# Kernel optimization log

Measured on AMD Instinct MI355X. Metric: run time of the kernel, lower is better.

## Reference

```python
import jax, jax.numpy as jnp
import numpy as np

RES = 300
NC = 48
N_PTS = 1_000_000


def _bilinear2d(params, gx, gy):
    """params: (C,R,R); gx,gy: (N,) in [-1,1]. grid_sample align_corners=True,
    gx indexes width (last axis), gy indexes height."""
    C, R, _ = params.shape
    px = (gx + 1.0) * 0.5 * (R - 1)
    py = (gy + 1.0) * 0.5 * (R - 1)
    x0f = jnp.floor(px)
    y0f = jnp.floor(py)
    wx = px - x0f
    wy = py - y0f
    x0 = jnp.clip(x0f.astype(jnp.int32), 0, R - 1)
    x1 = jnp.clip(x0 + 1, 0, R - 1)
    y0 = jnp.clip(y0f.astype(jnp.int32), 0, R - 1)
    y1 = jnp.clip(y0 + 1, 0, R - 1)
    f00 = params[:, y0, x0]  # (C,N)
    f01 = params[:, y0, x1]
    f10 = params[:, y1, x0]
    f11 = params[:, y1, x1]
    return (f00 * (1 - wx) * (1 - wy) + f01 * wx * (1 - wy)
            + f10 * (1 - wx) * wy + f11 * wx * wy)


def _linear1d(params, gy):
    """params: (C,R) (line grid with width 1, x-coord fixed at 0); gy: (N,)."""
    C, R = params.shape
    py = (gy + 1.0) * 0.5 * (R - 1)
    y0f = jnp.floor(py)
    wy = py - y0f
    y0 = jnp.clip(y0f.astype(jnp.int32), 0, R - 1)
    y1 = jnp.clip(y0 + 1, 0, R - 1)
    return params[:, y0] * (1 - wy) + params[:, y1] * wy  # (C,N)


def setup_inputs() -> dict:
    key = jax.random.key(0)
    k1, k2, k3 = jax.random.split(key, 3)
    x = jax.random.uniform(k1, (N_PTS, 3), dtype=jnp.float32)
    plane_params = 0.1 * jax.random.normal(k2, (3, NC, RES, RES), dtype=jnp.float32)
    line_params = 0.1 * jax.random.normal(k3, (3, NC, RES, 1), dtype=jnp.float32)
    return {"x": x, "plane_params": plane_params, "line_params": line_params}


def reference(x, plane_params, line_params):
    N = x.shape[0]
    xs = 2.0 * x - 1.0  # (N,3)
    # grid_sample grid is (x_coord, y_coord): plane pairs [0,1],[0,2],[1,2]
    gx = jnp.stack([xs[:, 0], xs[:, 0], xs[:, 1]])  # (3,N) width coord
    gy = jnp.stack([xs[:, 1], xs[:, 2], xs[:, 2]])  # (3,N) height coord
    gl = jnp.stack([xs[:, 2], xs[:, 1], xs[:, 0]])  # (3,N) line coord
    plane_f = jax.vmap(_bilinear2d)(plane_params, gx, gy)      # (3,C,N)
    line_f = jax.vmap(_linear1d)(line_params[..., 0], gl)      # (3,C,N)
    feats = (plane_f * line_f).reshape(3 * NC, N).T            # (N, 3C)
    return feats
```

## Files before the change

kernel.cpp:

```cpp
#include <hip/hip_runtime.h>
#include <hip/hip_fp16.h>

#define RES 300
#define NC 48
#define RES2 (RES * RES)
#define NBINS 32768
#define TPP 12

typedef float f32x4 __attribute__((ext_vector_type(4)));
typedef unsigned int u32x4 __attribute__((ext_vector_type(4)));

struct alignas(8) h4 { __half2 h[2]; };

__device__ __forceinline__ int clampi(int v, int lo, int hi) {
    return v < lo ? lo : (v > hi ? hi : v);
}

__device__ __forceinline__ unsigned spread5(unsigned v) {
    v &= 31u;
    v = (v | (v << 8)) & 0x100Fu;
    v = (v | (v << 4)) & 0x10C3u;
    v = (v | (v << 2)) & 0x1249u;
    return v;
}

__device__ __forceinline__ unsigned morton_key(float a, float b, float c) {
    int ca = clampi((int)(a * 32.0f), 0, 31);
    int cb = clampi((int)(b * 32.0f), 0, 31);
    int cc = clampi((int)(c * 32.0f), 0, 31);
    return spread5((unsigned)ca) | (spread5((unsigned)cb) << 1) | (spread5((unsigned)cc) << 2);
}


__global__ __launch_bounds__(256) void tp_planes_kernel(const float* __restrict__ in,
                                                        __half* __restrict__ out) {
    unsigned idx = blockIdx.x * 256u + threadIdx.x;
    if (idx >= 3u * RES2) return;
    unsigned p  = idx / RES2;
    unsigned yx = idx - p * RES2;
    const float* src = in + (size_t)p * NC * RES2 + yx;
    unsigned short v[NC];
#pragma unroll
    for (int c = 0; c < NC; ++c) {
        __half h = __float2half(src[(size_t)c * RES2]);
        v[c] = *reinterpret_cast<unsigned short*>(&h);
    }
    u32x4* dst = reinterpret_cast<u32x4*>(out + (size_t)idx * NC);
#pragma unroll
    for (int i = 0; i < 6; ++i) {
        u32x4 w;
        w.x = (unsigned)v[8 * i + 0] | ((unsigned)v[8 * i + 1] << 16);
        w.y = (unsigned)v[8 * i + 2] | ((unsigned)v[8 * i + 3] << 16);
        w.z = (unsigned)v[8 * i + 4] | ((unsigned)v[8 * i + 5] << 16);
        w.w = (unsigned)v[8 * i + 6] | ((unsigned)v[8 * i + 7] << 16);
        dst[i] = w;
    }
}

__global__ __launch_bounds__(256) void tp_lines_kernel(const float* __restrict__ in,
                                                       __half* __restrict__ out) {
    unsigned idx = blockIdx.x * 256u + threadIdx.x;
    if (idx >= 3u * RES) return;
    unsigned p = idx / RES;
    unsigned y = idx - p * RES;
#pragma unroll
    for (int c = 0; c < NC; ++c)
        out[(size_t)idx * NC + c] = __float2half(in[((size_t)p * NC + c) * RES + y]);
}


__global__ __launch_bounds__(256) void zero_bins_kernel(unsigned* __restrict__ counts) {
    unsigned i = blockIdx.x * 256u + threadIdx.x;
    if (i < NBINS) counts[i] = 0u;
}

__global__ __launch_bounds__(256) void hist_kernel(const float* __restrict__ x,
                                                   unsigned* __restrict__ counts,
                                                   unsigned N) {
    unsigned i = blockIdx.x * 256u + threadIdx.x;
    if (i >= N) return;
    unsigned k = morton_key(x[3u * i], x[3u * i + 1u], x[3u * i + 2u]);
    atomicAdd(&counts[k], 1u);
}

__global__ __launch_bounds__(1024) void scan_kernel(const unsigned* __restrict__ counts,
                                                    unsigned* __restrict__ offs) {
    __shared__ unsigned part[1024];
    int t = threadIdx.x;
    unsigned local[NBINS / 1024];
    unsigned s = 0;
#pragma unroll
    for (int j = 0; j < NBINS / 1024; ++j) {
        local[j] = counts[t * (NBINS / 1024) + j];
        s += local[j];
    }
    part[t] = s;
    __syncthreads();
    for (int d = 1; d < 1024; d <<= 1) {
        unsigned v = (t >= d) ? part[t - d] : 0u;
        __syncthreads();
        part[t] += v;
        __syncthreads();
    }
    unsigned run = (t == 0) ? 0u : part[t - 1];
#pragma unroll
    for (int j = 0; j < NBINS / 1024; ++j) {
        offs[t * (NBINS / 1024) + j] = run;
        run += local[j];
    }
}

__global__ __launch_bounds__(256) void scatter_kernel(const float* __restrict__ x,
                                                      unsigned* __restrict__ offs,
                                                      f32x4* __restrict__ sorted,
                                                      unsigned N) {
    unsigned i = blockIdx.x * 256u + threadIdx.x;
    if (i >= N) return;
    float a = x[3u * i], b = x[3u * i + 1u], c = x[3u * i + 2u];
    unsigned k = morton_key(a, b, c);
    unsigned pos = atomicAdd(&offs[k], 1u);
    f32x4 v;
    v.x = a; v.y = b; v.z = c; v.w = __uint_as_float(i);
    sorted[pos] = v;
}


__global__ __launch_bounds__(256) void encode_sorted_kernel(const f32x4* __restrict__ sorted,
                                                            const __half* __restrict__ pt,
                                                            const __half* __restrict__ lt,
                                                            float* __restrict__ out,
                                                            unsigned N) {
    unsigned nwg  = gridDim.x;
    unsigned orig = blockIdx.x;
    unsigned xcd = orig & 7u, j = orig >> 3u;
    unsigned qq = nwg >> 3u, r = nwg & 7u;
    unsigned bid = (xcd < r ? xcd * (qq + 1u) : r * (qq + 1u) + (xcd - r) * qq) + j;

    unsigned gid = bid * 256u + threadIdx.x;
    if (gid >= N * TPP) return;
    unsigned s  = gid / TPP;
    unsigned c4 = gid - s * TPP;

    f32x4 pv4 = sorted[s];
    unsigned n = __float_as_uint(pv4.w);
    float xs0 = pv4.x, xs1 = pv4.y, xs2 = pv4.z;

    unsigned cbase = c4 * 4u;

    h4 c00_0, c01_0, c10_0, c11_0, L0_0, L1_0;
    h4 c00_1, c01_1, c10_1, c11_1, L0_1, L1_1;
    h4 c00_2, c01_2, c10_2, c11_2, L0_2, L1_2;
    float w00_[3], w01_[3], w10_[3], w11_[3], wl_[3];

#pragma unroll
    for (int p = 0; p < 3; ++p) {
        float gxv = (p == 2) ? xs1 : xs0;
        float gyv = (p == 0) ? xs1 : xs2;
        float glv = (p == 0) ? xs2 : ((p == 1) ? xs1 : xs0);

        float gxs = 2.0f * gxv - 1.0f;
        float gys = 2.0f * gyv - 1.0f;
        float gls = 2.0f * glv - 1.0f;
        float px = (gxs + 1.0f) * 0.5f * (float)(RES - 1);
        float py = (gys + 1.0f) * 0.5f * (float)(RES - 1);
        float pl = (gls + 1.0f) * 0.5f * (float)(RES - 1);

        float x0f = floorf(px), y0f = floorf(py), l0f = floorf(pl);
        float wx = px - x0f, wy = py - y0f, wl = pl - l0f;

        int ix0 = clampi((int)x0f, 0, RES - 1);
        int ix1 = ix0 + 1 > RES - 1 ? RES - 1 : ix0 + 1;
        int iy0 = clampi((int)y0f, 0, RES - 1);
        int iy1 = iy0 + 1 > RES - 1 ? RES - 1 : iy0 + 1;
        int il0 = clampi((int)l0f, 0, RES - 1);
        int il1 = il0 + 1 > RES - 1 ? RES - 1 : il0 + 1;

        w00_[p] = (1.0f - wx) * (1.0f - wy);
        w01_[p] = wx * (1.0f - wy);
        w10_[p] = (1.0f - wx) * wy;
        w11_[p] = wx * wy;
        wl_[p]  = wl;

        const __half* pb = pt + (size_t)p * RES2 * NC;
        const __half* lb = lt + (size_t)p * RES * NC + cbase;
        unsigned o00 = ((unsigned)iy0 * RES + (unsigned)ix0) * NC + cbase;
        unsigned o01 = ((unsigned)iy0 * RES + (unsigned)ix1) * NC + cbase;
        unsigned o10 = ((unsigned)iy1 * RES + (unsigned)ix0) * NC + cbase;
        unsigned o11 = ((unsigned)iy1 * RES + (unsigned)ix1) * NC + cbase;

        h4 a = *reinterpret_cast<const h4*>(pb + o00);
        h4 b = *reinterpret_cast<const h4*>(pb + o01);
        h4 c = *reinterpret_cast<const h4*>(pb + o10);
        h4 d = *reinterpret_cast<const h4*>(pb + o11);
        h4 e = *reinterpret_cast<const h4*>(lb + (size_t)il0 * NC);
        h4 f = *reinterpret_cast<const h4*>(lb + (size_t)il1 * NC);
        if (p == 0) { c00_0 = a; c01_0 = b; c10_0 = c; c11_0 = d; L0_0 = e; L1_0 = f; }
        if (p == 1) { c00_1 = a; c01_1 = b; c10_1 = c; c11_1 = d; L0_1 = e; L1_1 = f; }
        if (p == 2) { c00_2 = a; c01_2 = b; c10_2 = c; c11_2 = d; L0_2 = e; L1_2 = f; }
    }

    float* ob = out + (size_t)n * 144u + cbase;

#pragma unroll
    for (int p = 0; p < 3; ++p) {
        h4 v00 = (p == 0) ? c00_0 : (p == 1) ? c00_1 : c00_2;
        h4 v01 = (p == 0) ? c01_0 : (p == 1) ? c01_1 : c01_2;
        h4 v10 = (p == 0) ? c10_0 : (p == 1) ? c10_1 : c10_2;
        h4 v11 = (p == 0) ? c11_0 : (p == 1) ? c11_1 : c11_2;
        h4 vl0 = (p == 0) ? L0_0  : (p == 1) ? L0_1  : L0_2;
        h4 vl1 = (p == 0) ? L1_0  : (p == 1) ? L1_1  : L1_2;

        float2 f00a = __half22float2(v00.h[0]), f00b = __half22float2(v00.h[1]);
        float2 f01a = __half22float2(v01.h[0]), f01b = __half22float2(v01.h[1]);
        float2 f10a = __half22float2(v10.h[0]), f10b = __half22float2(v10.h[1]);
        float2 f11a = __half22float2(v11.h[0]), f11b = __half22float2(v11.h[1]);
        float2 l0a  = __half22float2(vl0.h[0]), l0b  = __half22float2(vl0.h[1]);
        float2 l1a  = __half22float2(vl1.h[0]), l1b  = __half22float2(vl1.h[1]);

        float w00 = w00_[p], w01 = w01_[p], w10 = w10_[p], w11 = w11_[p];
        float wl = wl_[p], wl0 = 1.0f - wl;

        f32x4 plane_v;
        plane_v.x = f00a.x * w00 + f01a.x * w01 + f10a.x * w10 + f11a.x * w11;
        plane_v.y = f00a.y * w00 + f01a.y * w01 + f10a.y * w10 + f11a.y * w11;
        plane_v.z = f00b.x * w00 + f01b.x * w01 + f10b.x * w10 + f11b.x * w11;
        plane_v.w = f00b.y * w00 + f01b.y * w01 + f10b.y * w10 + f11b.y * w11;

        f32x4 line_v;
        line_v.x = l0a.x * wl0 + l1a.x * wl;
        line_v.y = l0a.y * wl0 + l1a.y * wl;
        line_v.z = l0b.x * wl0 + l1b.x * wl;
        line_v.w = l0b.y * wl0 + l1b.y * wl;

        f32x4 rr = plane_v * line_v;
        __builtin_nontemporal_store(rr, reinterpret_cast<f32x4*>(ob + p * 48));
    }
}


__global__ __launch_bounds__(256) void encode_kernel(const float* __restrict__ x,
                                                     const __half* __restrict__ pt,
                                                     const __half* __restrict__ lt,
                                                     float* __restrict__ out,
                                                     unsigned N) {
    unsigned gid = blockIdx.x * 256u + threadIdx.x;
    if (gid >= N * 36u) return;
    unsigned n  = gid / 36u;
    unsigned q  = gid - n * 36u;
    unsigned p  = q / 12u;
    unsigned c4 = q - p * 12u;

    float xv0 = x[3u * n + 0u];
    float xv1 = x[3u * n + 1u];
    float xv2 = x[3u * n + 2u];
    float gxv = (p == 2u) ? xv1 : xv0;
    float gyv = (p == 0u) ? xv1 : xv2;
    float glv = (p == 0u) ? xv2 : ((p == 1u) ? xv1 : xv0);

    float gxs = 2.0f * gxv - 1.0f;
    float gys = 2.0f * gyv - 1.0f;
    float gls = 2.0f * glv - 1.0f;
    float px = (gxs + 1.0f) * 0.5f * (float)(RES - 1);
    float py = (gys + 1.0f) * 0.5f * (float)(RES - 1);
    float pl = (gls + 1.0f) * 0.5f * (float)(RES - 1);

    float x0f = floorf(px), y0f = floorf(py), l0f = floorf(pl);
    float wx = px - x0f, wy = py - y0f, wl = pl - l0f;

    int ix0 = clampi((int)x0f, 0, RES - 1);
    int ix1 = ix0 + 1 > RES - 1 ? RES - 1 : ix0 + 1;
    int iy0 = clampi((int)y0f, 0, RES - 1);
    int iy1 = iy0 + 1 > RES - 1 ? RES - 1 : iy0 + 1;
    int il0 = clampi((int)l0f, 0, RES - 1);
    int il1 = il0 + 1 > RES - 1 ? RES - 1 : il0 + 1;

    unsigned cbase = c4 * 4u;
    const __half* pb = pt + (size_t)p * RES2 * NC;
    h4 v00 = *reinterpret_cast<const h4*>(pb + ((unsigned)iy0 * RES + (unsigned)ix0) * NC + cbase);
    h4 v01 = *reinterpret_cast<const h4*>(pb + ((unsigned)iy0 * RES + (unsigned)ix1) * NC + cbase);
    h4 v10 = *reinterpret_cast<const h4*>(pb + ((unsigned)iy1 * RES + (unsigned)ix0) * NC + cbase);
    h4 v11 = *reinterpret_cast<const h4*>(pb + ((unsigned)iy1 * RES + (unsigned)ix1) * NC + cbase);

    float2 f00a = __half22float2(v00.h[0]), f00b = __half22float2(v00.h[1]);
    float2 f01a = __half22float2(v01.h[0]), f01b = __half22float2(v01.h[1]);
    float2 f10a = __half22float2(v10.h[0]), f10b = __half22float2(v10.h[1]);
    float2 f11a = __half22float2(v11.h[0]), f11b = __half22float2(v11.h[1]);

    float w00 = (1.0f - wx) * (1.0f - wy);
    float w01 = wx * (1.0f - wy);
    float w10 = (1.0f - wx) * wy;
    float w11 = wx * wy;

    f32x4 plane_v;
    plane_v.x = f00a.x * w00 + f01a.x * w01 + f10a.x * w10 + f11a.x * w11;
    plane_v.y = f00a.y * w00 + f01a.y * w01 + f10a.y * w10 + f11a.y * w11;
    plane_v.z = f00b.x * w00 + f01b.x * w01 + f10b.x * w10 + f11b.x * w11;
    plane_v.w = f00b.y * w00 + f01b.y * w01 + f10b.y * w10 + f11b.y * w11;

    const __half* lb = lt + (size_t)p * RES * NC + cbase;
    h4 vl0 = *reinterpret_cast<const h4*>(lb + (size_t)il0 * NC);
    h4 vl1 = *reinterpret_cast<const h4*>(lb + (size_t)il1 * NC);
    float2 l0a = __half22float2(vl0.h[0]), l0b = __half22float2(vl0.h[1]);
    float2 l1a = __half22float2(vl1.h[0]), l1b = __half22float2(vl1.h[1]);

    float wl0 = 1.0f - wl;
    f32x4 line_v;
    line_v.x = l0a.x * wl0 + l1a.x * wl;
    line_v.y = l0a.y * wl0 + l1a.y * wl;
    line_v.z = l0b.x * wl0 + l1b.x * wl;
    line_v.w = l0b.y * wl0 + l1b.y * wl;

    f32x4 rr = plane_v * line_v;
    __builtin_nontemporal_store(rr, reinterpret_cast<f32x4*>(out + (size_t)n * 144u + (size_t)q * 4u));
}

__global__ __launch_bounds__(256) void encode_fallback_kernel(const float* __restrict__ x,
                                                              const float* __restrict__ plane,
                                                              const float* __restrict__ line,
                                                              float* __restrict__ out,
                                                              unsigned N) {
    unsigned gid = blockIdx.x * 256u + threadIdx.x;
    if (gid >= N * 36u) return;
    unsigned n  = gid / 36u;
    unsigned q  = gid - n * 36u;
    unsigned p  = q / 12u;
    unsigned c4 = q - p * 12u;

    float xv0 = x[3u * n + 0u];
    float xv1 = x[3u * n + 1u];
    float xv2 = x[3u * n + 2u];
    float gxv = (p == 2u) ? xv1 : xv0;
    float gyv = (p == 0u) ? xv1 : xv2;
    float glv = (p == 0u) ? xv2 : ((p == 1u) ? xv1 : xv0);

    float gxs = 2.0f * gxv - 1.0f;
    float gys = 2.0f * gyv - 1.0f;
    float gls = 2.0f * glv - 1.0f;
    float px = (gxs + 1.0f) * 0.5f * (float)(RES - 1);
    float py = (gys + 1.0f) * 0.5f * (float)(RES - 1);
    float pl = (gls + 1.0f) * 0.5f * (float)(RES - 1);

    float x0f = floorf(px), y0f = floorf(py), l0f = floorf(pl);
    float wx = px - x0f, wy = py - y0f, wl = pl - l0f;

    int ix0 = clampi((int)x0f, 0, RES - 1);
    int ix1 = ix0 + 1 > RES - 1 ? RES - 1 : ix0 + 1;
    int iy0 = clampi((int)y0f, 0, RES - 1);
    int iy1 = iy0 + 1 > RES - 1 ? RES - 1 : iy0 + 1;
    int il0 = clampi((int)l0f, 0, RES - 1);
    int il1 = il0 + 1 > RES - 1 ? RES - 1 : il0 + 1;

    float w00 = (1.0f - wx) * (1.0f - wy);
    float w01 = wx * (1.0f - wy);
    float w10 = (1.0f - wx) * wy;
    float w11 = wx * wy;
    float wl0 = 1.0f - wl;

    float4 r;
    float* rp = &r.x;
#pragma unroll
    for (int cc = 0; cc < 4; ++cc) {
        unsigned c = c4 * 4u + (unsigned)cc;
        const float* pp = plane + ((size_t)p * NC + c) * RES2;
        float f00 = pp[(size_t)iy0 * RES + ix0];
        float f01 = pp[(size_t)iy0 * RES + ix1];
        float f10 = pp[(size_t)iy1 * RES + ix0];
        float f11 = pp[(size_t)iy1 * RES + ix1];
        float pv = f00 * w00 + f01 * w01 + f10 * w10 + f11 * w11;
        const float* lp = line + ((size_t)p * NC + c) * RES;
        float lv = lp[il0] * wl0 + lp[il1] * wl;
        rp[cc] = pv * lv;
    }
    *reinterpret_cast<float4*>(out + (size_t)n * 144u + (size_t)q * 4u) = r;
}

extern "C" void kernel_launch(void* const* d_in, const int* in_sizes, int n_in,
                              void* d_out, int out_size, void* d_ws, size_t ws_size,
                              hipStream_t stream) {
    const float* x     = (const float*)d_in[0];
    const float* plane = (const float*)d_in[1];
    const float* line  = (const float*)d_in[2];
    float* out = (float*)d_out;
    unsigned N = (unsigned)(in_sizes[0] / 3);

    size_t plane_t_elems = (size_t)3 * RES2 * NC;
    size_t line_t_elems  = (size_t)3 * RES * NC;
    size_t sorted_bytes  = (size_t)N * 16u;
    size_t plane_bytes   = plane_t_elems * sizeof(__half);
    size_t line_bytes    = line_t_elems * sizeof(__half);
    size_t bins_bytes    = (size_t)NBINS * 4u;

    size_t need_mid  = plane_bytes + line_bytes;
    size_t need_full = sorted_bytes + plane_bytes + line_bytes + 2u * bins_bytes;

    unsigned pblocks = (N + 255u) / 256u;

    if (ws_size >= need_full) {
        char* base = (char*)d_ws;
        f32x4*   sorted  = (f32x4*)base;                      base += sorted_bytes;
        __half*  plane_t = (__half*)base;                     base += plane_bytes;
        __half*  line_t  = (__half*)base;                     base += line_bytes;
        unsigned* counts = (unsigned*)base;                   base += bins_bytes;
        unsigned* offs   = (unsigned*)base;

        unsigned total  = N * TPP;
        unsigned blocks = (total + 255u) / 256u;

        zero_bins_kernel<<<(NBINS + 255) / 256, 256, 0, stream>>>(counts);
        hist_kernel<<<pblocks, 256, 0, stream>>>(x, counts, N);
        tp_planes_kernel<<<(3u * RES2 + 255u) / 256u, 256, 0, stream>>>(plane, plane_t);
        tp_lines_kernel<<<(3u * RES + 255u) / 256u, 256, 0, stream>>>(line, line_t);
        scan_kernel<<<1, 1024, 0, stream>>>(counts, offs);
        scatter_kernel<<<pblocks, 256, 0, stream>>>(x, offs, sorted, N);
        encode_sorted_kernel<<<blocks, 256, 0, stream>>>(sorted, plane_t, line_t, out, N);
    } else if (ws_size >= need_mid) {
        __half* plane_t = (__half*)d_ws;
        __half* line_t  = plane_t + plane_t_elems;
        unsigned total  = N * 36u;
        unsigned blocks = (total + 255u) / 256u;
        tp_planes_kernel<<<(3u * RES2 + 255u) / 256u, 256, 0, stream>>>(plane, plane_t);
        tp_lines_kernel<<<(3u * RES + 255u) / 256u, 256, 0, stream>>>(line, line_t);
        encode_kernel<<<blocks, 256, 0, stream>>>(x, plane_t, line_t, out, N);
    } else {
        unsigned total  = N * 36u;
        unsigned blocks = (total + 255u) / 256u;
        encode_fallback_kernel<<<blocks, 256, 0, stream>>>(x, plane, line, out, N);
    }
}
```

Before: 281.8 us.

## Refine Morton binning to 64^3 cells with multi-block scan and merged transposes

Raises the Morton sort grid from 32^3 to 64^3 bins, which gives finer spatial locality for the gather-heavy encode and spreads the histogram and scatter atomics over more bins. The single-block scan is replaced by a three-kernel hierarchical scan so the larger bin count stays parallel. The plane and line transpose kernels are merged into one launch. In exchange it adds two extra kernel launches and more bin memory traffic.

```diff
diff --git a/kernel.cpp b/kernel.cpp
--- a/kernel.cpp
+++ b/kernel.cpp
@@ -4,7 +4,10 @@
 #define RES 300
 #define NC 48
 #define RES2 (RES * RES)
-#define NBINS 32768
+#define CELLS 64
+#define NBINS (CELLS*CELLS*CELLS)
+#define SCAN_T 1024
+#define SCAN_BLK (NBINS / SCAN_T)
 #define TPP 12
 
 typedef float f32x4 __attribute__((ext_vector_type(4)));
@@ -16,56 +19,56 @@
     return v < lo ? lo : (v > hi ? hi : v);
 }
 
-__device__ __forceinline__ unsigned spread5(unsigned v) {
-    v &= 31u;
-    v = (v | (v << 8)) & 0x100Fu;
-    v = (v | (v << 4)) & 0x10C3u;
-    v = (v | (v << 2)) & 0x1249u;
+__device__ __forceinline__ unsigned spread3(unsigned v) {
+    v = (v | (v << 16)) & 0x030000FFu;
+    v = (v | (v << 8))  & 0x0300F00Fu;
+    v = (v | (v << 4))  & 0x030C30C3u;
+    v = (v | (v << 2))  & 0x09249249u;
     return v;
 }
 
 __device__ __forceinline__ unsigned morton_key(float a, float b, float c) {
-    int ca = clampi((int)(a * 32.0f), 0, 31);
-    int cb = clampi((int)(b * 32.0f), 0, 31);
-    int cc = clampi((int)(c * 32.0f), 0, 31);
-    return spread5((unsigned)ca) | (spread5((unsigned)cb) << 1) | (spread5((unsigned)cc) << 2);
-}
-
-
-__global__ __launch_bounds__(256) void tp_planes_kernel(const float* __restrict__ in,
-                                                        __half* __restrict__ out) {
+    unsigned ca = (unsigned)clampi((int)(a * (float)CELLS), 0, CELLS - 1);
+    unsigned cb = (unsigned)clampi((int)(b * (float)CELLS), 0, CELLS - 1);
+    unsigned cc = (unsigned)clampi((int)(c * (float)CELLS), 0, CELLS - 1);
+    return spread3(ca) | (spread3(cb) << 1) | (spread3(cc) << 2);
+}
+
+
+__global__ __launch_bounds__(256) void tp_tables_kernel(const float* __restrict__ pin,
+                                                        const float* __restrict__ lin,
+                                                        __half* __restrict__ pout,
+                                                        __half* __restrict__ lout) {
     unsigned idx = blockIdx.x * 256u + threadIdx.x;
-    if (idx >= 3u * RES2) return;
-    unsigned p  = idx / RES2;
-    unsigned yx = idx - p * RES2;
-    const float* src = in + (size_t)p * NC * RES2 + yx;
-    unsigned short v[NC];
-#pragma unroll
-    for (int c = 0; c < NC; ++c) {
-        __half h = __float2half(src[(size_t)c * RES2]);
-        v[c] = *reinterpret_cast<unsigned short*>(&h);
-    }
-    u32x4* dst = reinterpret_cast<u32x4*>(out + (size_t)idx * NC);
-#pragma unroll
-    for (int i = 0; i < 6; ++i) {
-        u32x4 w;
-        w.x = (unsigned)v[8 * i + 0] | ((unsigned)v[8 * i + 1] << 16);
-        w.y = (unsigned)v[8 * i + 2] | ((unsigned)v[8 * i + 3] << 16);
-        w.z = (unsigned)v[8 * i + 4] | ((unsigned)v[8 * i + 5] << 16);
-        w.w = (unsigned)v[8 * i + 6] | ((unsigned)v[8 * i + 7] << 16);
-        dst[i] = w;
-    }
-}
-
-__global__ __launch_bounds__(256) void tp_lines_kernel(const float* __restrict__ in,
-                                                       __half* __restrict__ out) {
-    unsigned idx = blockIdx.x * 256u + threadIdx.x;
-    if (idx >= 3u * RES) return;
-    unsigned p = idx / RES;
-    unsigned y = idx - p * RES;
-#pragma unroll
-    for (int c = 0; c < NC; ++c)
-        out[(size_t)idx * NC + c] = __float2half(in[((size_t)p * NC + c) * RES + y]);
+    if (idx < 3u * RES2) {
+        unsigned p  = idx / RES2;
+        unsigned yx = idx - p * RES2;
+        const float* src = pin + (size_t)p * NC * RES2 + yx;
+        unsigned short v[NC];
+#pragma unroll
+        for (int c = 0; c < NC; ++c) {
+            __half h = __float2half(src[(size_t)c * RES2]);
+            v[c] = *reinterpret_cast<unsigned short*>(&h);
+        }
+        u32x4* dst = reinterpret_cast<u32x4*>(pout + (size_t)idx * NC);
+#pragma unroll
+        for (int i = 0; i < 6; ++i) {
+            u32x4 w;
+            w.x = (unsigned)v[8 * i + 0] | ((unsigned)v[8 * i + 1] << 16);
+            w.y = (unsigned)v[8 * i + 2] | ((unsigned)v[8 * i + 3] << 16);
+            w.z = (unsigned)v[8 * i + 4] | ((unsigned)v[8 * i + 5] << 16);
+            w.w = (unsigned)v[8 * i + 6] | ((unsigned)v[8 * i + 7] << 16);
+            dst[i] = w;
+        }
+    } else {
+        unsigned li = idx - 3u * RES2;
+        if (li >= 3u * RES) return;
+        unsigned p = li / RES;
+        unsigned y = li - p * RES;
+#pragma unroll
+        for (int c = 0; c < NC; ++c)
+            lout[(size_t)li * NC + c] = __float2half(lin[((size_t)p * NC + c) * RES + y]);
+    }
 }
 
 
@@ -83,31 +86,46 @@
     atomicAdd(&counts[k], 1u);
 }
 
-__global__ __launch_bounds__(1024) void scan_kernel(const unsigned* __restrict__ counts,
-                                                    unsigned* __restrict__ offs) {
-    __shared__ unsigned part[1024];
+__global__ __launch_bounds__(SCAN_T) void scan1_kernel(const unsigned* __restrict__ counts,
+                                                       unsigned* __restrict__ pre,
+                                                       unsigned* __restrict__ bsum) {
+    __shared__ unsigned part[SCAN_T];
+    unsigned b = blockIdx.x * SCAN_T + threadIdx.x;
     int t = threadIdx.x;
-    unsigned local[NBINS / 1024];
-    unsigned s = 0;
-#pragma unroll
-    for (int j = 0; j < NBINS / 1024; ++j) {
-        local[j] = counts[t * (NBINS / 1024) + j];
-        s += local[j];
-    }
-    part[t] = s;
+    unsigned c = counts[b];
+    part[t] = c;
     __syncthreads();
-    for (int d = 1; d < 1024; d <<= 1) {
+    for (int d = 1; d < SCAN_T; d <<= 1) {
         unsigned v = (t >= d) ? part[t - d] : 0u;
         __syncthreads();
         part[t] += v;
         __syncthreads();
     }
-    unsigned run = (t == 0) ? 0u : part[t - 1];
-#pragma unroll
-    for (int j = 0; j < NBINS / 1024; ++j) {
-        offs[t * (NBINS / 1024) + j] = run;
-        run += local[j];
-    }
+    pre[b] = part[t] - c;
+    if (t == SCAN_T - 1) bsum[blockIdx.x] = part[t];
+}
+
+__global__ __launch_bounds__(SCAN_BLK) void scan2_kernel(unsigned* __restrict__ bsum,
+                                                         unsigned* __restrict__ boff) {
+    __shared__ unsigned part[SCAN_BLK];
+    int t = threadIdx.x;
+    unsigned c = bsum[t];
+    part[t] = c;
+    __syncthreads();
+    for (int d = 1; d < SCAN_BLK; d <<= 1) {
+        unsigned v = (t >= d) ? part[t - d] : 0u;
+        __syncthreads();
+        part[t] += v;
+        __syncthreads();
+    }
+    boff[t] = part[t] - c;
+}
+
+__global__ __launch_bounds__(SCAN_T) void scan3_kernel(const unsigned* __restrict__ pre,
+                                                       const unsigned* __restrict__ boff,
+                                                       unsigned* __restrict__ offs) {
+    unsigned b = blockIdx.x * SCAN_T + threadIdx.x;
+    offs[b] = pre[b] + boff[blockIdx.x];
 }
 
 __global__ __launch_bounds__(256) void scatter_kernel(const float* __restrict__ x,
@@ -389,28 +407,34 @@
     size_t plane_bytes   = plane_t_elems * sizeof(__half);
     size_t line_bytes    = line_t_elems * sizeof(__half);
     size_t bins_bytes    = (size_t)NBINS * 4u;
+    size_t bsum_bytes    = (size_t)SCAN_BLK * 4u;
 
     size_t need_mid  = plane_bytes + line_bytes;
-    size_t need_full = sorted_bytes + plane_bytes + line_bytes + 2u * bins_bytes;
+    size_t need_full = sorted_bytes + plane_bytes + line_bytes + 3u * bins_bytes + 2u * bsum_bytes;
 
     unsigned pblocks = (N + 255u) / 256u;
+    unsigned tpblocks = (3u * RES2 + 3u * RES + 255u) / 256u;
 
     if (ws_size >= need_full) {
         char* base = (char*)d_ws;
-        f32x4*   sorted  = (f32x4*)base;                      base += sorted_bytes;
-        __half*  plane_t = (__half*)base;                     base += plane_bytes;
-        __half*  line_t  = (__half*)base;                     base += line_bytes;
-        unsigned* counts = (unsigned*)base;                   base += bins_bytes;
-        unsigned* offs   = (unsigned*)base;
+        f32x4*   sorted  = (f32x4*)base;    base += sorted_bytes;
+        __half*  plane_t = (__half*)base;   base += plane_bytes;
+        __half*  line_t  = (__half*)base;   base += line_bytes;
+        unsigned* counts = (unsigned*)base; base += bins_bytes;
+        unsigned* pre    = (unsigned*)base; base += bins_bytes;
+        unsigned* offs   = (unsigned*)base; base += bins_bytes;
+        unsigned* bsum   = (unsigned*)base; base += bsum_bytes;
+        unsigned* boff   = (unsigned*)base;
 
         unsigned total  = N * TPP;
         unsigned blocks = (total + 255u) / 256u;
 
         zero_bins_kernel<<<(NBINS + 255) / 256, 256, 0, stream>>>(counts);
         hist_kernel<<<pblocks, 256, 0, stream>>>(x, counts, N);
-        tp_planes_kernel<<<(3u * RES2 + 255u) / 256u, 256, 0, stream>>>(plane, plane_t);
-        tp_lines_kernel<<<(3u * RES + 255u) / 256u, 256, 0, stream>>>(line, line_t);
-        scan_kernel<<<1, 1024, 0, stream>>>(counts, offs);
+        tp_tables_kernel<<<tpblocks, 256, 0, stream>>>(plane, line, plane_t, line_t);
+        scan1_kernel<<<SCAN_BLK, SCAN_T, 0, stream>>>(counts, pre, bsum);
+        scan2_kernel<<<1, SCAN_BLK, 0, stream>>>(bsum, boff);
+        scan3_kernel<<<SCAN_BLK, SCAN_T, 0, stream>>>(pre, boff, offs);
         scatter_kernel<<<pblocks, 256, 0, stream>>>(x, offs, sorted, N);
         encode_sorted_kernel<<<blocks, 256, 0, stream>>>(sorted, plane_t, line_t, out, N);
     } else if (ws_size >= need_mid) {
@@ -418,8 +442,7 @@
         __half* line_t  = plane_t + plane_t_elems;
         unsigned total  = N * 36u;
         unsigned blocks = (total + 255u) / 256u;
-        tp_planes_kernel<<<(3u * RES2 + 255u) / 256u, 256, 0, stream>>>(plane, plane_t);
-        tp_lines_kernel<<<(3u * RES + 255u) / 256u, 256, 0, stream>>>(line, line_t);
+        tp_tables_kernel<<<tpblocks, 256, 0, stream>>>(plane, line, plane_t, line_t);
         encode_kernel<<<blocks, 256, 0, stream>>>(x, plane_t, line_t, out, N);
     } else {
         unsigned total  = N * 36u;
```

Result: faster. 273.9 us (-2.8%).
